# Kernel tuning notes

Hardware: AMD Instinct MI355X
Metric: run time of the kernel (lower is better)

The kernel has to match this reference:

```python
import jax, jax.numpy as jnp
import numpy as np

B = 256
H, W = 8, 16          # input_resolution for channels=256
C = 768               # dim = channels*3
WS = 4                # window_size
SHIFT = 2             # shift_size
NH = 12               # num_heads
HD = C // NH          # head_dim = 64
HID = 1024            # mlp hidden = channels*4
N = WS * WS           # tokens per window = 16
NW = (H // WS) * (W // WS)  # windows per image = 8
LN_EPS = 1e-5


def _rel_pos_index():
    coords = np.stack(np.meshgrid(np.arange(WS), np.arange(WS), indexing='ij'))  # [2,ws,ws]
    cf = coords.reshape(2, -1)                      # [2, N]
    rel = (cf[:, :, None] - cf[:, None, :]).transpose(1, 2, 0)  # [N, N, 2]
    rel[:, :, 0] += WS - 1
    rel[:, :, 1] += WS - 1
    rel[:, :, 0] *= 2 * WS - 1
    return jnp.asarray(rel.sum(-1))                 # [N, N] int


def _attn_mask():
    img = np.zeros((H, W))
    slices = (slice(0, -WS), slice(-WS, -SHIFT), slice(-SHIFT, None))
    cnt = 0
    for hs in slices:
        for ws_ in slices:
            img[hs, ws_] = cnt
            cnt += 1
    mw = img.reshape(H // WS, WS, W // WS, WS).transpose(0, 2, 1, 3).reshape(-1, N)  # [nW, N]
    am = mw[:, None, :] - mw[:, :, None]            # [nW, N, N]
    return jnp.asarray(np.where(am != 0, -100.0, 0.0).astype(np.float32))


REL_IDX = _rel_pos_index()
ATTN_MASK = _attn_mask()


def _ln(x, g, b):
    m = x.mean(-1, keepdims=True)
    v = ((x - m) ** 2).mean(-1, keepdims=True)
    return (x - m) / jnp.sqrt(v + LN_EPS) * g + b


def setup_inputs() -> dict:
    key = jax.random.key(0)
    ks = jax.random.split(key, 8)
    s = 0.02
    return {
        'x': jax.random.normal(ks[0], (B, H * W, C), jnp.float32),
        'ln1_g': jnp.ones((C,), jnp.float32),
        'ln1_b': jnp.zeros((C,), jnp.float32),
        'qkv_w': jax.random.normal(ks[1], (C, 3 * C), jnp.float32) * s,
        'qkv_b': jnp.zeros((3 * C,), jnp.float32),
        'proj_w': jax.random.normal(ks[2], (C, C), jnp.float32) * s,
        'proj_b': jnp.zeros((C,), jnp.float32),
        'rel_table': jax.random.normal(ks[3], ((2 * WS - 1) * (2 * WS - 1), NH), jnp.float32) * s,
        'ln2_g': jnp.ones((C,), jnp.float32),
        'ln2_b': jnp.zeros((C,), jnp.float32),
        'fc1_w': jax.random.normal(ks[4], (C, HID), jnp.float32) * s,
        'fc1_b': jax.random.normal(ks[5], (HID,), jnp.float32) * 1e-6,
        'fc2_w': jax.random.normal(ks[6], (HID, C), jnp.float32) * s,
        'fc2_b': jax.random.normal(ks[7], (C,), jnp.float32) * 1e-6,
    }


def reference(x, ln1_g, ln1_b, qkv_w, qkv_b, proj_w, proj_b, rel_table,
              ln2_g, ln2_b, fc1_w, fc1_b, fc2_w, fc2_b):
    # --- norm1 + cyclic shift + window partition ---
    h = _ln(x, ln1_g, ln1_b).reshape(B, H, W, C)
    h = jnp.roll(h, (-SHIFT, -SHIFT), axis=(1, 2))
    hw = h.reshape(B, H // WS, WS, W // WS, WS, C).transpose(0, 1, 3, 2, 4, 5)
    hw = hw.reshape(B * NW, N, C)                   # (num_windows*B, N, C)
    # --- window attention with relative position bias + shift mask ---
    qkv = (hw @ qkv_w + qkv_b).reshape(B * NW, N, 3, NH, HD).transpose(2, 0, 3, 1, 4)
    q, k, v = qkv[0] * (HD ** -0.5), qkv[1], qkv[2]  # [Bn, NH, N, HD]
    attn = jnp.einsum('bhnd,bhmd->bhnm', q, k)      # [Bn, NH, N, N]
    bias = rel_table[REL_IDX].transpose(2, 0, 1)    # [NH, N, N]
    attn = attn + bias[None]
    attn = attn.reshape(B, NW, NH, N, N) + ATTN_MASK[None, :, None]
    attn = jax.nn.softmax(attn.reshape(B * NW, NH, N, N), axis=-1)
    o = jnp.einsum('bhnm,bhmd->bhnd', attn, v).transpose(0, 2, 1, 3).reshape(B * NW, N, C)
    o = o @ proj_w + proj_b
    # --- window reverse + reverse shift + residual ---
    o = o.reshape(B, H // WS, W // WS, WS, WS, C).transpose(0, 1, 3, 2, 4, 5).reshape(B, H, W, C)
    o = jnp.roll(o, (SHIFT, SHIFT), axis=(1, 2)).reshape(B, H * W, C)
    x = x + o
    # --- MLP block (dropout is identity at inference) ---
    y = _ln(x, ln2_g, ln2_b)
    y = jax.nn.gelu(y @ fc1_w + fc1_b, approximate=False)
    return x + (y @ fc2_w + fc2_b)
```

## Files before the change

kernel.cpp:

```cpp
#include <hip/hip_runtime.h>
#include <stdint.h>
#include <stddef.h>

typedef __attribute__((ext_vector_type(8))) short bf16x8;
typedef __attribute__((ext_vector_type(4))) float f32x4;
typedef __attribute__((ext_vector_type(4))) unsigned int uint4v;

static __device__ __forceinline__ unsigned short f2bf(float f) {
  unsigned int u = __builtin_bit_cast(unsigned int, f);
  unsigned int r = (u + 0x7FFFu + ((u >> 16) & 1u)) >> 16;
  return (unsigned short)r;
}

static __device__ __forceinline__ void gld16(const void* g, void* l) {
  __builtin_amdgcn_global_load_lds(
      (const __attribute__((address_space(1))) void*)g,
      (__attribute__((address_space(3))) void*)l, 16, 0, 0);
}

__global__ void transpose_cast(const float* __restrict__ src,
                               unsigned short* __restrict__ dst, int R, int C) {
  __shared__ float tile[32][33];
  int c0 = blockIdx.x * 32, r0 = blockIdx.y * 32;
  int tx = threadIdx.x, ty = threadIdx.y;
  #pragma unroll
  for (int i = 0; i < 32; i += 8)
    tile[ty + i][tx] = src[(size_t)(r0 + ty + i) * C + c0 + tx];
  __syncthreads();
  #pragma unroll
  for (int i = 0; i < 32; i += 8)
    dst[(size_t)(c0 + ty + i) * R + r0 + tx] = f2bf(tile[tx][ty + i]);
}

static __device__ __forceinline__ float blksum256(float v, float* sb) {
  #pragma unroll
  for (int o = 32; o > 0; o >>= 1) v += __shfl_down(v, o, 64);
  int lane = threadIdx.x & 63, w = threadIdx.x >> 6;
  __syncthreads();
  if (lane == 0) sb[w] = v;
  __syncthreads();
  return sb[0] + sb[1] + sb[2] + sb[3];
}

template <int MODE>
__global__ __launch_bounds__(256) void ln_kernel(const float* __restrict__ x,
                                                 const float* __restrict__ gg,
                                                 const float* __restrict__ bb,
                                                 unsigned short* __restrict__ out) {
  __shared__ float sb[4];
  const int d = blockIdx.x;
  size_t srow;
  if (MODE == 0) {
    int b = d >> 7, wid = (d >> 4) & 7, tok = d & 15;
    int oh = (((wid >> 2) << 2) + (tok >> 2) + 2) & 7;
    int ow = (((wid & 3) << 2) + (tok & 3) + 2) & 15;
    srow = (size_t)(b << 7) + oh * 16 + ow;
  } else {
    srow = d;
  }
  const float* xr = x + srow * 768;
  const int t = threadIdx.x;
  float v0 = xr[t], v1 = xr[t + 256], v2 = xr[t + 512];
  float mean = blksum256(v0 + v1 + v2, sb) * (1.0f / 768.0f);
  float d0 = v0 - mean, d1 = v1 - mean, d2 = v2 - mean;
  float var = blksum256(d0 * d0 + d1 * d1 + d2 * d2, sb) * (1.0f / 768.0f);
  float rstd = rsqrtf(var + 1e-5f);
  size_t o = (size_t)d * 768;
  out[o + t]       = f2bf(d0 * rstd * gg[t] + bb[t]);
  out[o + t + 256] = f2bf(d1 * rstd * gg[t + 256] + bb[t + 256]);
  out[o + t + 512] = f2bf(d2 * rstd * gg[t + 512] + bb[t + 512]);
}

template <int EPI>
__global__ __launch_bounds__(512, 2) void gemm256(
    const unsigned short* __restrict__ A, const unsigned short* __restrict__ BT,
    const float* __restrict__ bias, float* __restrict__ outF,
    unsigned short* __restrict__ outB, const float* __restrict__ resid,
    int M, int N, int K, int NT) {
  __shared__ __align__(16) unsigned short sA[2][256 * 64];
  __shared__ __align__(16) unsigned short sB[2][256 * 64];

  const int tid = threadIdx.x;
  const int lane = tid & 63, wv = tid >> 6;
  const int wr = wv >> 2, wc = wv & 3;
  const int fr = lane & 15, q4 = (lane >> 4) << 2;

  const int nwg = gridDim.x;
  const int orig = blockIdx.x;
  const int swz = (orig & 7) * (nwg >> 3) + (orig >> 3);
  const int mt = swz / NT, nt = swz - mt * NT;
  const int m0 = mt << 8, n0 = nt << 8;

  const size_t K2 = (size_t)K * 2;

  const int srow = tid >> 3;
  const int sg = tid & 7;
  const int sgs = ((sg ^ (srow & 7)) << 4);
  const char* pA = (const char*)A + (size_t)(m0 + srow) * K2 + sgs;
  const char* pB = (const char*)BT + (size_t)(n0 + srow) * K2 + sgs;
  char* sdA = (char*)&sA[0][0] + (wv << 10);
  char* sdB = (char*)&sB[0][0] + (wv << 10);

  const int g0 = (((lane >> 4) ^ (fr & 7)) << 4);
  const int g1 = (((4 + (lane >> 4)) ^ (fr & 7)) << 4);
  const int arow = (wr << 7) + fr;
  const int brow = (wc << 6) + fr;

  f32x4 acc[8][4];
  #pragma unroll
  for (int i = 0; i < 8; ++i)
    #pragma unroll
    for (int j = 0; j < 4; ++j) acc[i][j] = (f32x4){0.f, 0.f, 0.f, 0.f};

  bf16x8 af[4][2];
  bf16x8 bbv[2][2][2];
  const int KT = K >> 6;
  const int NI = KT >> 1;

#define BARR __builtin_amdgcn_s_barrier()
#define VM8 asm volatile("s_waitcnt vmcnt(8)" ::: "memory")
#define VM0 asm volatile("s_waitcnt vmcnt(0)" ::: "memory")

#define LDA(CB, mh)                                                          \
  {                                                                          \
    const char* ba = ((const char*)&sA[0][0]) + (CB)*32768;                  \
    _Pragma("unroll") for (int fm = 0; fm < 4; ++fm) {                       \
      const int r = arow + (mh)*64 + fm * 16;                                \
      af[fm][0] = *(const bf16x8*)(ba + r * 128 + g0);                       \
      af[fm][1] = *(const bf16x8*)(ba + r * 128 + g1);                       \
    }                                                                        \
  }
#define LDB(CB, nh)                                                          \
  {                                                                          \
    const char* ba = ((const char*)&sB[0][0]) + (CB)*32768;                  \
    _Pragma("unroll") for (int fn = 0; fn < 2; ++fn) {                       \
      const int r = brow + (nh)*32 + fn * 16;                                \
      bbv[nh][fn][0] = *(const bf16x8*)(ba + r * 128 + g0);                  \
      bbv[nh][fn][1] = *(const bf16x8*)(ba + r * 128 + g1);                  \
    }                                                                        \
  }
#define STGA(CB, tt, j)                                                      \
  gld16(pA + (size_t)((j)*64) * K2 + ((size_t)(tt) << 7),                    \
        sdA + (CB)*32768 + (j)*8192);
#define STGB(CB, tt, j)                                                      \
  gld16(pB + (size_t)((j)*64) * K2 + ((size_t)(tt) << 7),                    \
        sdB + (CB)*32768 + (j)*8192);
#define MMAQ(mh, nh)                                                         \
  _Pragma("unroll") for (int fm = 0; fm < 4; ++fm)                           \
      _Pragma("unroll") for (int fn = 0; fn < 2; ++fn) {                     \
    f32x4* ac = &acc[(mh)*4 + fm][(nh)*2 + fn];                              \
    *ac = __builtin_amdgcn_mfma_f32_16x16x32_bf16(af[fm][0], bbv[nh][fn][0], \
                                                  *ac, 0, 0, 0);             \
    *ac = __builtin_amdgcn_mfma_f32_16x16x32_bf16(af[fm][1], bbv[nh][fn][1], \
                                                  *ac, 0, 0, 0);             \
  }
#define OPEN  BARR; __builtin_amdgcn_s_setprio(1)
#define CLOSE __builtin_amdgcn_s_setprio(0)

  #pragma unroll
  for (int j = 0; j < 4; ++j) { STGA(0, 0, j); STGB(0, 0, j); }
  #pragma unroll
  for (int j = 0; j < 4; ++j) { STGA(1, 1, j); STGB(1, 1, j); }
  VM8;
  BARR;

  for (int i = 0; i < NI; ++i) {
    const int s2 = 2 * i + 2, s3 = 2 * i + 3;
    const bool gl = (i + 1 < NI);
    LDB(0, 0) LDA(0, 0)
    OPEN; MMAQ(0, 0); CLOSE; BARR;
    LDB(0, 1)
    if (gl) { STGA(0, s2, 0); STGA(0, s2, 2); }
    OPEN; MMAQ(0, 1); CLOSE; BARR;
    LDA(0, 1)
    if (gl) { STGB(0, s2, 0); STGB(0, s2, 1); }
    OPEN; MMAQ(1, 1); CLOSE; BARR;
    if (gl) { STGA(0, s2, 1); STGA(0, s2, 3); STGB(0, s2, 2); STGB(0, s2, 3); }
    OPEN; MMAQ(1, 0); CLOSE;
    if (gl) { VM8; } else { VM0; }
    BARR;
    LDB(1, 0) LDA(1, 0)
    OPEN; MMAQ(0, 0); CLOSE; BARR;
    LDB(1, 1)
    if (gl) { STGA(1, s3, 0); STGA(1, s3, 2); }
    OPEN; MMAQ(0, 1); CLOSE; BARR;
    LDA(1, 1)
    if (gl) { STGB(1, s3, 0); STGB(1, s3, 1); }
    OPEN; MMAQ(1, 1); CLOSE; BARR;
    if (gl) { STGA(1, s3, 1); STGA(1, s3, 3); STGB(1, s3, 2); STGB(1, s3, 3); }
    OPEN; MMAQ(1, 0); CLOSE;
    if (gl) { VM8; }
    BARR;
  }
#undef BARR
#undef VM8
#undef VM0
#undef LDA
#undef LDB
#undef STGA
#undef STGB
#undef MMAQ
#undef OPEN
#undef CLOSE

  #pragma unroll
  for (int ai = 0; ai < 8; ++ai) {
    #pragma unroll
    for (int bj = 0; bj < 4; ++bj) {
      const int col = n0 + (wc << 6) + bj * 16 + fr;
      const float bc = bias[col];
      #pragma unroll
      for (int i = 0; i < 4; ++i) {
        const int row = m0 + (wr << 7) + ai * 16 + q4 + i;
        float v = acc[ai][bj][i] + bc;
        if (EPI == 0) {
          outB[(size_t)row * N + col] = f2bf(v);
        } else if (EPI == 1) {
          int b = row >> 7, wid = (row >> 4) & 7, tok = row & 15;
          int oh = (((wid >> 2) << 2) + (tok >> 2) + 2) & 7;
          int ow = (((wid & 3) << 2) + (tok & 3) + 2) & 15;
          size_t di = ((size_t)(b << 7) + oh * 16 + ow) * 768 + col;
          outF[di] = v + resid[di];
        } else if (EPI == 2) {
          float g = 0.5f * v * (1.0f + erff(v * 0.70710678118f));
          outB[(size_t)row * N + col] = f2bf(g);
        } else {
          size_t di = (size_t)row * N + col;
          outF[di] = v + resid[di];
        }
      }
    }
  }
}

__global__ __launch_bounds__(64) void attn_win(const unsigned short* __restrict__ qkv,
                                               const float* __restrict__ rel_table,
                                               unsigned short* __restrict__ o) {
  __shared__ __align__(16) unsigned short q_s[16 * 64];
  __shared__ __align__(16) unsigned short k_s[16 * 64];
  __shared__ __align__(16) unsigned short vt_s[64 * 32];
  __shared__ __align__(16) unsigned short p_s[16 * 32];
  const int bid = blockIdx.x;
  const int win = bid / 12;
  const int head = bid - win * 12;
  const int wid = win & 7;
  const int lane = threadIdx.x;
  const unsigned short* gq =
      qkv + (size_t)win * 16 * 2304 + head * 64 + (size_t)(lane >> 2) * 2304 + ((lane & 3) << 4);
  const int t = lane >> 2, d0 = (lane & 3) << 4;
  *(uint4v*)&q_s[t * 64 + d0]     = *(const uint4v*)(gq);
  *(uint4v*)&q_s[t * 64 + d0 + 8] = *(const uint4v*)(gq + 8);
  *(uint4v*)&k_s[t * 64 + d0]     = *(const uint4v*)(gq + 768);
  *(uint4v*)&k_s[t * 64 + d0 + 8] = *(const uint4v*)(gq + 776);
  unsigned short vv[16];
  *(uint4v*)&vv[0] = *(const uint4v*)(gq + 1536);
  *(uint4v*)&vv[8] = *(const uint4v*)(gq + 1544);
  #pragma unroll
  for (int e = 0; e < 16; ++e) vt_s[(d0 + e) * 32 + t] = vv[e];
  #pragma unroll
  for (int e = 0; e < 16; ++e) vt_s[lane * 32 + 16 + e] = 0;
  if (lane < 16) {
    #pragma unroll
    for (int e = 0; e < 16; ++e) p_s[lane * 32 + 16 + e] = 0;
  }
  __syncthreads();

  const int fr = lane & 15, kg = (lane >> 4) << 3;
  bf16x8 qa0 = *(const bf16x8*)&q_s[fr * 64 + kg];
  bf16x8 qa1 = *(const bf16x8*)&q_s[fr * 64 + 32 + kg];
  bf16x8 ka0 = *(const bf16x8*)&k_s[fr * 64 + kg];
  bf16x8 ka1 = *(const bf16x8*)&k_s[fr * 64 + 32 + kg];
  f32x4 s = (f32x4){0.f, 0.f, 0.f, 0.f};
  s = __builtin_amdgcn_mfma_f32_16x16x32_bf16(qa0, ka0, s, 0, 0, 0);
  s = __builtin_amdgcn_mfma_f32_16x16x32_bf16(qa1, ka1, s, 0, 0, 0);

  const int wh = wid >> 2, wwc = wid & 3;
  const int rj = fr >> 2, cj = fr & 3;
  const int rowm = wh * 4 + rj, colm = wwc * 4 + cj;
  const int rgm = (rowm < 4 ? 0 : (rowm < 6 ? 1 : 2)) * 3 +
                  (colm < 12 ? 0 : (colm < 14 ? 1 : 2));
  float p[4];
  #pragma unroll
  for (int i = 0; i < 4; ++i) {
    int n = ((lane >> 4) << 2) + i;
    int ri = n >> 2, ci = n & 3;
    int rown = wh * 4 + ri, coln = wwc * 4 + ci;
    int rgn = (rown < 4 ? 0 : (rown < 6 ? 1 : 2)) * 3 +
              (coln < 12 ? 0 : (coln < 14 ? 1 : 2));
    float bias = rel_table[(size_t)((ri - rj + 3) * 7 + (ci - cj + 3)) * 12 + head];
    p[i] = s[i] * 0.125f + bias + (rgn != rgm ? -100.0f : 0.0f);
  }
  float mx[4] = {p[0], p[1], p[2], p[3]};
  #pragma unroll
  for (int off = 8; off > 0; off >>= 1)
    #pragma unroll
    for (int i = 0; i < 4; ++i) mx[i] = fmaxf(mx[i], __shfl_xor(mx[i], off, 64));
  float sm[4];
  #pragma unroll
  for (int i = 0; i < 4; ++i) { p[i] = __expf(p[i] - mx[i]); sm[i] = p[i]; }
  #pragma unroll
  for (int off = 8; off > 0; off >>= 1)
    #pragma unroll
    for (int i = 0; i < 4; ++i) sm[i] += __shfl_xor(sm[i], off, 64);
  #pragma unroll
  for (int i = 0; i < 4; ++i)
    p_s[(((lane >> 4) << 2) + i) * 32 + fr] = f2bf(p[i] / sm[i]);
  __syncthreads();

  bf16x8 pa = *(const bf16x8*)&p_s[fr * 32 + kg];
  const f32x4 oz = (f32x4){0.f, 0.f, 0.f, 0.f};
  #pragma unroll
  for (int c = 0; c < 4; ++c) {
    bf16x8 vb = *(const bf16x8*)&vt_s[(c * 16 + fr) * 32 + kg];
    f32x4 oa = __builtin_amdgcn_mfma_f32_16x16x32_bf16(pa, vb, oz, 0, 0, 0);
    #pragma unroll
    for (int i = 0; i < 4; ++i) {
      int n = ((lane >> 4) << 2) + i;
      o[((size_t)win * 16 + n) * 768 + head * 64 + c * 16 + fr] = f2bf(oa[i]);
    }
  }
}

extern "C" void kernel_launch(void* const* d_in, const int* in_sizes, int n_in,
                              void* d_out, int out_size, void* d_ws, size_t ws_size,
                              hipStream_t stream) {
  const float* x      = (const float*)d_in[0];
  const float* ln1_g  = (const float*)d_in[1];
  const float* ln1_b  = (const float*)d_in[2];
  const float* qkv_w  = (const float*)d_in[3];
  const float* qkv_b  = (const float*)d_in[4];
  const float* proj_w = (const float*)d_in[5];
  const float* proj_b = (const float*)d_in[6];
  const float* rel_t  = (const float*)d_in[7];
  const float* ln2_g  = (const float*)d_in[8];
  const float* ln2_b  = (const float*)d_in[9];
  const float* fc1_w  = (const float*)d_in[10];
  const float* fc1_b  = (const float*)d_in[11];
  const float* fc2_w  = (const float*)d_in[12];
  const float* fc2_b  = (const float*)d_in[13];
  float* out = (float*)d_out;

  char* ws = (char*)d_ws;
  unsigned short* wsA = (unsigned short*)(ws);
  unsigned short* qkvb = (unsigned short*)(ws + 50331648);
  float* xr = (float*)(ws + 50331648);
  unsigned short* h1 = (unsigned short*)(ws + 201326592);
  unsigned short* qkv_wT = (unsigned short*)(ws + 268435456);
  unsigned short* proj_wT = (unsigned short*)(ws + 271974400);
  unsigned short* fc1_wT = (unsigned short*)(ws + 273154048);
  unsigned short* fc2_wT = (unsigned short*)(ws + 274726912);

  dim3 tb(32, 8);
  transpose_cast<<<dim3(2304 / 32, 768 / 32), tb, 0, stream>>>(qkv_w, qkv_wT, 768, 2304);
  transpose_cast<<<dim3(768 / 32, 768 / 32), tb, 0, stream>>>(proj_w, proj_wT, 768, 768);
  transpose_cast<<<dim3(1024 / 32, 768 / 32), tb, 0, stream>>>(fc1_w, fc1_wT, 768, 1024);
  transpose_cast<<<dim3(768 / 32, 1024 / 32), tb, 0, stream>>>(fc2_w, fc2_wT, 1024, 768);

  ln_kernel<0><<<32768, 256, 0, stream>>>(x, ln1_g, ln1_b, wsA);
  gemm256<0><<<dim3(128 * 9), 512, 0, stream>>>(wsA, qkv_wT, qkv_b, nullptr, qkvb,
                                                nullptr, 32768, 2304, 768, 9);
  attn_win<<<24576, 64, 0, stream>>>(qkvb, rel_t, wsA);
  gemm256<1><<<dim3(128 * 3), 512, 0, stream>>>(wsA, proj_wT, proj_b, xr, nullptr,
                                                x, 32768, 768, 768, 3);
  ln_kernel<1><<<32768, 256, 0, stream>>>(xr, ln2_g, ln2_b, wsA);
  gemm256<2><<<dim3(128 * 4), 512, 0, stream>>>(wsA, fc1_wT, fc1_b, nullptr, h1,
                                                nullptr, 32768, 1024, 768, 4);
  gemm256<3><<<dim3(128 * 3), 512, 0, stream>>>(h1, fc2_wT, fc2_b, out, nullptr,
                                                xr, 32768, 768, 1024, 3);
}
```

Measured before the change: 543.6 us.

## Store intermediate residual in bf16 and rebalance GEMM prefetch schedule

The post-attention residual stream is now kept in bf16 instead of fp32. The proj GEMM epilogue writes bf16, LN2 reads bf16, and the fc2 epilogue reads the bf16 residual, which halves that tensor's traffic across three kernels. Separately, the GEMM main loop issues part of the A-tile global-to-LDS loads later, adjusts vmcnt waits from 8 to 6, and adds an lgkmcnt(0) wait before each MFMA block. The bf16 residual loses precision in the skip connection, and the reordered prefetch changes how much latency stays hidden.

```diff
diff --git a/kernel.cpp b/kernel.cpp
--- a/kernel.cpp
+++ b/kernel.cpp
@@ -10,6 +10,10 @@
   unsigned int u = __builtin_bit_cast(unsigned int, f);
   unsigned int r = (u + 0x7FFFu + ((u >> 16) & 1u)) >> 16;
   return (unsigned short)r;
+}
+static __device__ __forceinline__ float bf2f(unsigned short h) {
+  unsigned int u = ((unsigned int)h) << 16;
+  return __builtin_bit_cast(float, u);
 }
 
 static __device__ __forceinline__ void gld16(const void* g, void* l) {
@@ -43,7 +47,8 @@
 }
 
 template <int MODE>
-__global__ __launch_bounds__(256) void ln_kernel(const float* __restrict__ x,
+__global__ __launch_bounds__(256) void ln_kernel(const float* __restrict__ xf,
+                                                 const unsigned short* __restrict__ xb,
                                                  const float* __restrict__ gg,
                                                  const float* __restrict__ bb,
                                                  unsigned short* __restrict__ out) {
@@ -58,9 +63,15 @@
   } else {
     srow = d;
   }
-  const float* xr = x + srow * 768;
   const int t = threadIdx.x;
-  float v0 = xr[t], v1 = xr[t + 256], v2 = xr[t + 512];
+  float v0, v1, v2;
+  if (MODE == 0) {
+    const float* xr_ = xf + srow * 768;
+    v0 = xr_[t]; v1 = xr_[t + 256]; v2 = xr_[t + 512];
+  } else {
+    const unsigned short* xr_ = xb + srow * 768;
+    v0 = bf2f(xr_[t]); v1 = bf2f(xr_[t + 256]); v2 = bf2f(xr_[t + 512]);
+  }
   float mean = blksum256(v0 + v1 + v2, sb) * (1.0f / 768.0f);
   float d0 = v0 - mean, d1 = v1 - mean, d2 = v2 - mean;
   float var = blksum256(d0 * d0 + d1 * d1 + d2 * d2, sb) * (1.0f / 768.0f);
@@ -76,6 +87,7 @@
     const unsigned short* __restrict__ A, const unsigned short* __restrict__ BT,
     const float* __restrict__ bias, float* __restrict__ outF,
     unsigned short* __restrict__ outB, const float* __restrict__ resid,
+    const unsigned short* __restrict__ residB,
     int M, int N, int K, int NT) {
   __shared__ __align__(16) unsigned short sA[2][256 * 64];
   __shared__ __align__(16) unsigned short sB[2][256 * 64];
@@ -118,7 +130,8 @@
   const int NI = KT >> 1;
 
 #define BARR __builtin_amdgcn_s_barrier()
-#define VM8 asm volatile("s_waitcnt vmcnt(8)" ::: "memory")
+#define LGKM0 asm volatile("s_waitcnt lgkmcnt(0)" ::: "memory")
+#define VM6 asm volatile("s_waitcnt vmcnt(6)" ::: "memory")
 #define VM0 asm volatile("s_waitcnt vmcnt(0)" ::: "memory")
 
 #define LDA(CB, mh)                                                          \
@@ -154,20 +167,21 @@
     *ac = __builtin_amdgcn_mfma_f32_16x16x32_bf16(af[fm][1], bbv[nh][fn][1], \
                                                   *ac, 0, 0, 0);             \
   }
-#define OPEN  BARR; __builtin_amdgcn_s_setprio(1)
+#define OPEN  BARR; LGKM0; __builtin_amdgcn_s_setprio(1)
 #define CLOSE __builtin_amdgcn_s_setprio(0)
 
   #pragma unroll
   for (int j = 0; j < 4; ++j) { STGA(0, 0, j); STGB(0, 0, j); }
-  #pragma unroll
-  for (int j = 0; j < 4; ++j) { STGA(1, 1, j); STGB(1, 1, j); }
-  VM8;
+  STGA(1, 1, 0); STGA(1, 1, 2);
+  STGB(1, 1, 0); STGB(1, 1, 1); STGB(1, 1, 2); STGB(1, 1, 3);
+  VM6;
   BARR;
 
   for (int i = 0; i < NI; ++i) {
-    const int s2 = 2 * i + 2, s3 = 2 * i + 3;
+    const int s1 = 2 * i + 1, s2 = 2 * i + 2, s3 = 2 * i + 3;
     const bool gl = (i + 1 < NI);
     LDB(0, 0) LDA(0, 0)
+    STGA(1, s1, 1); STGA(1, s1, 3);
     OPEN; MMAQ(0, 0); CLOSE; BARR;
     LDB(0, 1)
     if (gl) { STGA(0, s2, 0); STGA(0, s2, 2); }
@@ -175,11 +189,12 @@
     LDA(0, 1)
     if (gl) { STGB(0, s2, 0); STGB(0, s2, 1); }
     OPEN; MMAQ(1, 1); CLOSE; BARR;
-    if (gl) { STGA(0, s2, 1); STGA(0, s2, 3); STGB(0, s2, 2); STGB(0, s2, 3); }
+    if (gl) { STGB(0, s2, 2); STGB(0, s2, 3); }
     OPEN; MMAQ(1, 0); CLOSE;
-    if (gl) { VM8; } else { VM0; }
+    if (gl) { VM6; } else { VM0; }
     BARR;
     LDB(1, 0) LDA(1, 0)
+    if (gl) { STGA(0, s2, 1); STGA(0, s2, 3); }
     OPEN; MMAQ(0, 0); CLOSE; BARR;
     LDB(1, 1)
     if (gl) { STGA(1, s3, 0); STGA(1, s3, 2); }
@@ -187,13 +202,14 @@
     LDA(1, 1)
     if (gl) { STGB(1, s3, 0); STGB(1, s3, 1); }
     OPEN; MMAQ(1, 1); CLOSE; BARR;
-    if (gl) { STGA(1, s3, 1); STGA(1, s3, 3); STGB(1, s3, 2); STGB(1, s3, 3); }
+    if (gl) { STGB(1, s3, 2); STGB(1, s3, 3); }
     OPEN; MMAQ(1, 0); CLOSE;
-    if (gl) { VM8; }
+    if (gl) { VM6; }
     BARR;
   }
 #undef BARR
-#undef VM8
+#undef LGKM0
+#undef VM6
 #undef VM0
 #undef LDA
 #undef LDB
@@ -220,13 +236,13 @@
           int oh = (((wid >> 2) << 2) + (tok >> 2) + 2) & 7;
           int ow = (((wid & 3) << 2) + (tok & 3) + 2) & 15;
           size_t di = ((size_t)(b << 7) + oh * 16 + ow) * 768 + col;
-          outF[di] = v + resid[di];
+          outB[di] = f2bf(v + resid[di]);
         } else if (EPI == 2) {
           float g = 0.5f * v * (1.0f + erff(v * 0.70710678118f));
           outB[(size_t)row * N + col] = f2bf(g);
         } else {
           size_t di = (size_t)row * N + col;
-          outF[di] = v + resid[di];
+          outF[di] = v + bf2f(residB[di]);
         }
       }
     }
@@ -343,7 +359,7 @@
   char* ws = (char*)d_ws;
   unsigned short* wsA = (unsigned short*)(ws);
   unsigned short* qkvb = (unsigned short*)(ws + 50331648);
-  float* xr = (float*)(ws + 50331648);
+  unsigned short* xr16 = (unsigned short*)(ws + 50331648);
   unsigned short* h1 = (unsigned short*)(ws + 201326592);
   unsigned short* qkv_wT = (unsigned short*)(ws + 268435456);
   unsigned short* proj_wT = (unsigned short*)(ws + 271974400);
@@ -356,15 +372,19 @@
   transpose_cast<<<dim3(1024 / 32, 768 / 32), tb, 0, stream>>>(fc1_w, fc1_wT, 768, 1024);
   transpose_cast<<<dim3(768 / 32, 1024 / 32), tb, 0, stream>>>(fc2_w, fc2_wT, 1024, 768);
 
-  ln_kernel<0><<<32768, 256, 0, stream>>>(x, ln1_g, ln1_b, wsA);
+  ln_kernel<0><<<32768, 256, 0, stream>>>(x, nullptr, ln1_g, ln1_b, wsA);
   gemm256<0><<<dim3(128 * 9), 512, 0, stream>>>(wsA, qkv_wT, qkv_b, nullptr, qkvb,
-                                                nullptr, 32768, 2304, 768, 9);
+                                                nullptr, nullptr,
+                                                32768, 2304, 768, 9);
   attn_win<<<24576, 64, 0, stream>>>(qkvb, rel_t, wsA);
-  gemm256<1><<<dim3(128 * 3), 512, 0, stream>>>(wsA, proj_wT, proj_b, xr, nullptr,
-                                                x, 32768, 768, 768, 3);
-  ln_kernel<1><<<32768, 256, 0, stream>>>(xr, ln2_g, ln2_b, wsA);
+  gemm256<1><<<dim3(128 * 3), 512, 0, stream>>>(wsA, proj_wT, proj_b, nullptr, xr16,
+                                                x, nullptr,
+                                                32768, 768, 768, 3);
+  ln_kernel<2><<<32768, 256, 0, stream>>>(nullptr, xr16, ln2_g, ln2_b, wsA);
   gemm256<2><<<dim3(128 * 4), 512, 0, stream>>>(wsA, fc1_wT, fc1_b, nullptr, h1,
-                                                nullptr, 32768, 1024, 768, 4);
+                                                nullptr, nullptr,
+                                                32768, 1024, 768, 4);
   gemm256<3><<<dim3(128 * 3), 512, 0, stream>>>(h1, fc2_wT, fc2_b, out, nullptr,
-                                                xr, 32768, 768, 1024, 3);
-}
+                                                nullptr, xr16,
+                                                32768, 768, 1024, 3);
+}
```

After: 513.0 us. 1.06x faster.
